# Kernel tuning notes

Measured on AMD Instinct MI355X. Metric: run time of the kernel, lower is better.

The kernel has to match this reference:

```python
import jax, jax.numpy as jnp
import numpy as np

NEG = -1e9  # finite stand-in for -inf so grads stay NaN-free
BLANK = 0

def _lse3(a, b, c):
    m = jnp.maximum(jnp.maximum(a, b), c)
    return m + jnp.log(jnp.exp(a - m) + jnp.exp(b - m) + jnp.exp(c - m))

def setup_inputs() -> dict:
    key = jax.random.key(0)
    k1, k2, k3, k4 = jax.random.split(key, 4)
    T, B, C, S = 1024, 128, 256, 128
    logits = jax.random.normal(k1, (T, B, C), dtype=jnp.float32)
    log_probs = jax.nn.log_softmax(logits, axis=-1)  # CTCLoss expects log-probs
    y = jax.random.randint(k2, (B, S), 1, C)                 # labels in [1, C), never blank
    input_lengths = jax.random.randint(k3, (B,), 768, T + 1)  # 768..T
    target_lengths = jax.random.randint(k4, (B,), 64, S + 1)  # 64..S
    return {"log_probs": log_probs, "y": y,
            "input_lengths": input_lengths, "target_lengths": target_lengths}

def _ctc_loss(log_probs, y, input_lengths, target_lengths):
    T, B, C = log_probs.shape
    S = y.shape[1]
    L = 2 * S + 1  # extended label sequence: blank, y1, blank, y2, ..., blank

    ext = jnp.zeros((B, L), dtype=y.dtype).at[:, 1::2].set(y)  # even slots = blank(0)
    pos = jnp.arange(L)
    prev2 = jnp.concatenate([jnp.full((B, 2), BLANK, dtype=ext.dtype), ext[:, :-2]], axis=1)
    allow_skip = (pos[None, :] >= 2) & (ext != BLANK) & (ext != prev2)  # [B, L]

    # init alpha at t=0: only s=0 (blank) and s=1 (first label) reachable
    lp0 = log_probs[0]  # [B, C]
    alpha0 = jnp.full((B, L), NEG, dtype=log_probs.dtype)
    alpha0 = alpha0.at[:, 0].set(lp0[:, BLANK])
    alpha0 = alpha0.at[:, 1].set(jnp.take_along_axis(lp0, ext[:, 1:2], axis=1)[:, 0])

    def step(alpha, xs):
        lp_t, t = xs  # lp_t: [B, C]
        a0 = alpha
        a1 = jnp.concatenate([jnp.full((B, 1), NEG, alpha.dtype), alpha[:, :-1]], axis=1)
        a2 = jnp.concatenate([jnp.full((B, 2), NEG, alpha.dtype), alpha[:, :-2]], axis=1)
        a2 = jnp.where(allow_skip, a2, NEG)
        emit = jnp.take_along_axis(lp_t, ext, axis=1)  # [B, L]
        new = _lse3(a0, a1, a2) + emit
        # freeze alpha for samples whose input has already ended
        new = jnp.where(t < input_lengths[:, None], new, alpha)
        return new, None

    ts = jnp.arange(1, T)
    alpha_T, _ = jax.lax.scan(step, alpha0, (log_probs[1:], ts))

    # final log-likelihood: logsumexp of alpha at positions 2*tl and 2*tl-1
    idx_hi = (2 * target_lengths)[:, None]       # [B,1]
    idx_lo = (2 * target_lengths - 1)[:, None]
    a_hi = jnp.take_along_axis(alpha_T, idx_hi, axis=1)[:, 0]
    a_lo = jnp.take_along_axis(alpha_T, idx_lo, axis=1)[:, 0]
    m = jnp.maximum(a_hi, a_lo)
    ll = m + jnp.log(jnp.exp(a_hi - m) + jnp.exp(a_lo - m))
    loss = -ll  # per-sample negative log-likelihood

    # zero_infinity=True: zero out infeasible (effectively -inf likelihood) samples
    loss = jnp.where(loss < 0.5 * (-NEG), loss, 0.0)

    # reduction='mean': divide each loss by its target length, then batch mean
    return jnp.mean(loss / target_lengths.astype(loss.dtype))

def reference(log_probs, y, input_lengths, target_lengths):
    return _ctc_loss(log_probs, y, input_lengths, target_lengths)
```

## Files before the change

kernel.cpp:

```cpp
#include <hip/hip_runtime.h>


#define CTC_C 256
#define RING 16
#define PFD  2

typedef unsigned int u32;

__device__ __forceinline__ void gll16(const void* g, void* l) {
  __builtin_amdgcn_global_load_lds(
      (const __attribute__((address_space(1))) u32*)g,
      (__attribute__((address_space(3))) u32*)l, 16, 0, 0);
}

__device__ __forceinline__ double wshr1_f64(double x) {
  int lo = __double2loint(x), hi = __double2hiint(x);
  lo = __builtin_amdgcn_update_dpp(0, lo, 0x138, 0xf, 0xf, true);
  hi = __builtin_amdgcn_update_dpp(0, hi, 0x138, 0xf, 0xf, true);
  return __hiloint2double(hi, lo);
}

template <int CTRL>
__device__ __forceinline__ unsigned dppmax(unsigned v) {
  unsigned t = (unsigned)__builtin_amdgcn_update_dpp(0, (int)v, CTRL, 0xf, 0xf, true);
  return v > t ? v : t;
}

__device__ __forceinline__ void renorm(double& Oa, double& Ob, double& Ea,
                                       double& Eb, double& E128, double& logC) {
  unsigned m =       (unsigned)__double2hiint(Oa);
  unsigned h;
  h = (unsigned)__double2hiint(Ob);   m = m > h ? m : h;
  h = (unsigned)__double2hiint(Ea);   m = m > h ? m : h;
  h = (unsigned)__double2hiint(Eb);   m = m > h ? m : h;
  h = (unsigned)__double2hiint(E128); m = m > h ? m : h;
  m = dppmax<0xB1>(m);
  m = dppmax<0x4E>(m);
  m = dppmax<0x141>(m);
  m = dppmax<0x140>(m);
  unsigned r0 = (unsigned)__builtin_amdgcn_readlane((int)m, 0);
  unsigned r1 = (unsigned)__builtin_amdgcn_readlane((int)m, 16);
  unsigned r2 = (unsigned)__builtin_amdgcn_readlane((int)m, 32);
  unsigned r3 = (unsigned)__builtin_amdgcn_readlane((int)m, 48);
  unsigned m01 = r0 > r1 ? r0 : r1;
  unsigned m23 = r2 > r3 ? r2 : r3;
  unsigned smax = m01 > m23 ? m01 : m23;
  int eb = (int)(smax >> 20);
  double s = __hiloint2double((int)((unsigned)(2045 - eb) << 20), 0);
  Oa *= s; Ob *= s; Ea *= s; Eb *= s; E128 *= s;
  logC += (double)(eb - 1022) * 0.6931471805599453;
}

__global__ __launch_bounds__(64)
void ctc_fwd(const float* __restrict__ lp, const int* __restrict__ y,
             const int* __restrict__ ilen, const int* __restrict__ tlen,
             float* __restrict__ out, int T, int B, int S) {
  __shared__ __align__(16) float ring[RING][CTC_C];

  const int b = blockIdx.x;
  const int l = threadIdx.x;
  const unsigned ROWB = (unsigned)(B * CTC_C * 4);

  const int len = ilen[b];
  const int tl  = tlen[b];

  const int ya = y[(size_t)b * S + 2 * l];
  const int yb = y[(size_t)b * S + 2 * l + 1];
  const int yprev = __shfl_up(yb, 1);
  const bool skipA = (l > 0) && (ya != yprev);
  const bool skipB = (yb != ya);

  const float* row0 = lp + (size_t)b * CTC_C;
  const int y0 = y[(size_t)b * S];
  double Ea = (l == 0) ? (double)__expf(row0[0])  : 0.;
  double Oa = (l == 0) ? (double)__expf(row0[y0]) : 0.;
  double Eb = 0., Ob = 0., E128 = 0., logC = 0.;

  const char* gLane = (const char*)lp + (size_t)b * CTC_C * 4 + 16 * (size_t)l;

  asm volatile("s_waitcnt vmcnt(0)" ::: "memory");
  __builtin_amdgcn_sched_barrier(0);

#pragma unroll
  for (int t = 1; t <= RING; ++t)
    gll16(gLane + (size_t)t * ROWB, &ring[t & 15][0]);
  asm volatile("s_waitcnt vmcnt(0)" ::: "memory");
  __builtin_amdgcn_sched_barrier(0);

  float pfA[2], pfB[2], pfQ[2];
  pfA[1] = ring[1][ya]; pfB[1] = ring[1][yb]; pfQ[1] = ring[1][0];
  pfA[0] = ring[2][ya]; pfB[0] = ring[2][yb]; pfQ[0] = ring[2][0];

  const unsigned capR = (unsigned)(T - 1) * ROWB;
  unsigned uoff = (unsigned)(RING + 1) * ROWB;

#define CTC_STEP(i_)                                                          \
  do {                                                                        \
    const int dp = (1 + (i_)) & 1;                   \
    const int sl = (3 + (i_)) & 15;                  \
    const int sg = (1 + (i_)) & 15;                \
    const double pa = (double)__expf(pfA[dp]);                                \
    const double pb = (double)__expf(pfB[dp]);                                \
    const double pq = (double)__expf(pfQ[dp]);                                \
    gll16(gLane + uoff, &ring[sg][0]);                                        \
    {                                                                         \
      unsigned un = uoff + ROWB;                                              \
      uoff = un < capR ? un : capR;                                           \
    }                                                                         \
    asm volatile("s_waitcnt vmcnt(14)" ::: "memory");                         \
    __builtin_amdgcn_sched_barrier(0);                                        \
    pfA[dp] = ring[sl][ya];                                                   \
    pfB[dp] = ring[sl][yb];                                                   \
    pfQ[dp] = ring[sl][0];                                                    \
    const double Opm1 = wshr1_f64(Ob);              \
    const double EaOp = Ea + Opm1;                                            \
    const double EbOa = Eb + Oa;                                              \
    const double tA = skipA ? EaOp : Ea;                                      \
    const double tB = skipB ? EbOa : Eb;                                      \
    const double nOa = (Oa + tA) * pa;                                        \
    const double nOb = (Ob + tB) * pb;                                        \
    Ea = EaOp * pq;                                                           \
    Eb = EbOa * pq;                                                           \
    E128 = (E128 + Ob) * pq;                        \
    Oa = nOa; Ob = nOb;                                                       \
    __builtin_amdgcn_sched_barrier(0);                                        \
  } while (0)

  const int nsteps = len - 1;
  const int nch = nsteps >> 4;
  const int rem = nsteps & 15;

  for (int c = 0; c < nch; ++c) {
#pragma unroll
    for (int i = 0; i < 16; ++i) {
      CTC_STEP(i);
      if ((i & 7) == 7) renorm(Oa, Ob, Ea, Eb, E128, logC);
    }
  }
  if (rem) {
#pragma unroll
    for (int i = 0; i < 16; ++i) {
      if (i < rem) {
        CTC_STEP(i);
        if ((i & 7) == 7) renorm(Oa, Ob, Ea, Eb, E128, logC);
      }
    }
  }
#undef CTC_STEP

  double vEa = __shfl(Ea, (tl >> 1) & 63);
  double vEb = __shfl(Eb, (tl >> 1) & 63);
  double vE128 = __shfl(E128, 63);
  double vhi = (tl == S) ? vE128 : ((tl & 1) ? vEb : vEa);
  const int s2 = tl - 1;
  double vOa = __shfl(Oa, (s2 >> 1) & 63);
  double vOb = __shfl(Ob, (s2 >> 1) & 63);
  double vlo = (s2 & 1) ? vOb : vOa;

  double sum = vhi + vlo;
  double loss;
  if (sum > 0.) {
    loss = -(logC + log(sum));
  } else {
    loss = 1e30;
  }
  if (!(loss < 5.0e8)) loss = 0.;
  float contrib = (float)(loss / (double)tl / (double)B);
  if (l == 0) atomicAdd(out, contrib);
}

extern "C" void kernel_launch(void* const* d_in, const int* in_sizes, int n_in,
                              void* d_out, int out_size, void* d_ws, size_t ws_size,
                              hipStream_t stream) {
  const float* lp   = (const float*)d_in[0];
  const int*   yy   = (const int*)d_in[1];
  const int*   ilen = (const int*)d_in[2];
  const int*   tlen = (const int*)d_in[3];
  float* out = (float*)d_out;

  int B = in_sizes[2];
  int S = in_sizes[1] / B;
  int T = in_sizes[0] / (B * CTC_C);

  hipMemsetAsync(out, 0, sizeof(float), stream);
  ctc_fwd<<<B, 64, 0, stream>>>(lp, yy, ilen, tlen, out, T, B, S);
}
```

Before: 258.7 us.

## Deepen LDS prefetch pipeline, software-pipeline exp, and reduce renorm frequency

Extends the register prefetch from a 2-deep to a 4-deep rotation and computes the exp of the emission probabilities one step ahead, so the transcendental and LDS reads stop sitting on the serial recurrence's critical path. It relaxes the vmcnt wait from 14 to 12 to match the deeper lookahead and drops the trailing sched_barrier so the compiler can interleave more freely. Renormalisation now runs once every 16 steps instead of every 8, and the cross-row max uses row_bcast DPP plus a single readlane instead of four readlanes. Renormalising less often leaves more room for double-precision underflow or overflow drift between rescales.

```diff
diff --git a/kernel.cpp b/kernel.cpp
--- a/kernel.cpp
+++ b/kernel.cpp
@@ -3,7 +3,6 @@
 
 #define CTC_C 256
 #define RING 16
-#define PFD  2
 
 typedef unsigned int u32;
 
@@ -38,13 +37,9 @@
   m = dppmax<0x4E>(m);
   m = dppmax<0x141>(m);
   m = dppmax<0x140>(m);
-  unsigned r0 = (unsigned)__builtin_amdgcn_readlane((int)m, 0);
-  unsigned r1 = (unsigned)__builtin_amdgcn_readlane((int)m, 16);
-  unsigned r2 = (unsigned)__builtin_amdgcn_readlane((int)m, 32);
-  unsigned r3 = (unsigned)__builtin_amdgcn_readlane((int)m, 48);
-  unsigned m01 = r0 > r1 ? r0 : r1;
-  unsigned m23 = r2 > r3 ? r2 : r3;
-  unsigned smax = m01 > m23 ? m01 : m23;
+  m = dppmax<0x142>(m);
+  m = dppmax<0x143>(m);
+  unsigned smax = (unsigned)__builtin_amdgcn_readlane((int)m, 63);
   int eb = (int)(smax >> 20);
   double s = __hiloint2double((int)((unsigned)(2045 - eb) << 20), 0);
   Oa *= s; Ob *= s; Ea *= s; Eb *= s; E128 *= s;
@@ -87,31 +82,43 @@
   asm volatile("s_waitcnt vmcnt(0)" ::: "memory");
   __builtin_amdgcn_sched_barrier(0);
 
-  float pfA[2], pfB[2], pfQ[2];
-  pfA[1] = ring[1][ya]; pfB[1] = ring[1][yb]; pfQ[1] = ring[1][0];
-  pfA[0] = ring[2][ya]; pfB[0] = ring[2][yb]; pfQ[0] = ring[2][0];
+  float pfA[4], pfB[4], pfQ[4];
+#pragma unroll
+  for (int t = 1; t <= 4; ++t) {
+    pfA[t & 3] = ring[t & 15][ya];
+    pfB[t & 3] = ring[t & 15][yb];
+    pfQ[t & 3] = ring[t & 15][0];
+  }
+  double eA2[2], eB2[2], eQ2[2];
+  eA2[1] = (double)__expf(pfA[1]);
+  eB2[1] = (double)__expf(pfB[1]);
+  eQ2[1] = (double)__expf(pfQ[1]);
 
   const unsigned capR = (unsigned)(T - 1) * ROWB;
   unsigned uoff = (unsigned)(RING + 1) * ROWB;
 
 #define CTC_STEP(i_)                                                          \
   do {                                                                        \
-    const int dp = (1 + (i_)) & 1;                   \
-    const int sl = (3 + (i_)) & 15;                  \
-    const int sg = (1 + (i_)) & 15;                \
-    const double pa = (double)__expf(pfA[dp]);                                \
-    const double pb = (double)__expf(pfB[dp]);                                \
-    const double pq = (double)__expf(pfQ[dp]);                                \
+    const int eu = (1 + (i_)) & 1;               \
+    const int en = (2 + (i_)) & 1;               \
+    const int pn = (2 + (i_)) & 3;               \
+    const int pr = (5 + (i_)) & 3;               \
+    const int sl = (5 + (i_)) & 15;              \
+    const int sg = (1 + (i_)) & 15;              \
+    const double pa = eA2[eu], pb = eB2[eu], pq = eQ2[eu];                    \
+    eA2[en] = (double)__expf(pfA[pn]);                                        \
+    eB2[en] = (double)__expf(pfB[pn]);                                        \
+    eQ2[en] = (double)__expf(pfQ[pn]);                                        \
     gll16(gLane + uoff, &ring[sg][0]);                                        \
     {                                                                         \
       unsigned un = uoff + ROWB;                                              \
       uoff = un < capR ? un : capR;                                           \
     }                                                                         \
-    asm volatile("s_waitcnt vmcnt(14)" ::: "memory");                         \
+    asm volatile("s_waitcnt vmcnt(12)" ::: "memory");                         \
     __builtin_amdgcn_sched_barrier(0);                                        \
-    pfA[dp] = ring[sl][ya];                                                   \
-    pfB[dp] = ring[sl][yb];                                                   \
-    pfQ[dp] = ring[sl][0];                                                    \
+    pfA[pr] = ring[sl][ya];                                                   \
+    pfB[pr] = ring[sl][yb];                                                   \
+    pfQ[pr] = ring[sl][0];                                                    \
     const double Opm1 = wshr1_f64(Ob);              \
     const double EaOp = Ea + Opm1;                                            \
     const double EbOa = Eb + Oa;                                              \
@@ -123,7 +130,6 @@
     Eb = EbOa * pq;                                                           \
     E128 = (E128 + Ob) * pq;                        \
     Oa = nOa; Ob = nOb;                                                       \
-    __builtin_amdgcn_sched_barrier(0);                                        \
   } while (0)
 
   const int nsteps = len - 1;
@@ -134,16 +140,13 @@
 #pragma unroll
     for (int i = 0; i < 16; ++i) {
       CTC_STEP(i);
-      if ((i & 7) == 7) renorm(Oa, Ob, Ea, Eb, E128, logC);
+      if (i == 15) renorm(Oa, Ob, Ea, Eb, E128, logC);
     }
   }
   if (rem) {
 #pragma unroll
     for (int i = 0; i < 16; ++i) {
-      if (i < rem) {
-        CTC_STEP(i);
-        if ((i & 7) == 7) renorm(Oa, Ob, Ea, Eb, E128, logC);
-      }
+      if (i < rem) CTC_STEP(i);
     }
   }
 #undef CTC_STEP
```

Measured after the change: 250.6 us. 3.1% less time.
